# Kernel tuning notes

Measured on AMD Instinct MI355X. Metric: run time of the kernel, lower is better.

Reference implementation:

```python
import jax, jax.numpy as jnp
import numpy as np

B, N, D, H = 2, 2048, 1024, 16
DH = D // H
DF = 4 * D
SCALE = D ** (-0.5)  # standard_scale=False -> dim**-0.5
EPS = 1e-5


def _ln(x, w, b):
    mu = jnp.mean(x, axis=-1, keepdims=True)
    var = jnp.mean(jnp.square(x - mu), axis=-1, keepdims=True)
    return (x - mu) * jax.lax.rsqrt(var + EPS) * w + b


def setup_inputs() -> dict:
    key = jax.random.key(0)
    ks = jax.random.split(key, 12)
    s = lambda fan_in: (1.0 / np.sqrt(fan_in))
    return {
        "x": jax.random.normal(ks[0], (B, N, D), jnp.float32),
        "gamma": jax.random.uniform(ks[1], (B, H), jnp.float32),
        "dist_matrix": jax.random.uniform(ks[2], (N, N), jnp.float32),
        "ln1_w": jnp.ones((D,), jnp.float32),
        "ln1_b": jnp.zeros((D,), jnp.float32),
        "qkv_w": jax.random.normal(ks[3], (D, 3 * D), jnp.float32) * s(D),
        "qkv_b": jnp.zeros((3 * D,), jnp.float32),
        "proj_w": jax.random.normal(ks[4], (D, D), jnp.float32) * s(D),
        "proj_b": jnp.zeros((D,), jnp.float32),
        "ln2_w": jnp.ones((D,), jnp.float32),
        "ln2_b": jnp.zeros((D,), jnp.float32),
        "mlp_w1": jax.random.normal(ks[5], (D, DF), jnp.float32) * s(D),
        "mlp_b1": jnp.zeros((DF,), jnp.float32),
        "mlp_w2": jax.random.normal(ks[6], (DF, D), jnp.float32) * s(DF),
        "mlp_b2": jnp.zeros((D,), jnp.float32),
    }


def reference(x, gamma, dist_matrix, ln1_w, ln1_b, qkv_w, qkv_b, proj_w, proj_b,
              ln2_w, ln2_b, mlp_w1, mlp_b1, mlp_w2, mlp_b2):
    # --- ZoomAttention on norm1(x) ---
    h = _ln(x, ln1_w, ln1_b)                                   # [B,N,D]
    qkv = h @ qkv_w + qkv_b                                    # [B,N,3D]
    qkv = qkv.reshape(B, N, 3, H, DH).transpose(2, 0, 3, 1, 4)  # [3,B,H,N,DH]
    q, k, v = qkv[0], qkv[1], qkv[2]
    scores = jnp.einsum("bhnd,bhmd->bhnm", q, k) * SCALE       # [B,H,N,N]
    scores = scores - gamma[:, :, None, None] * dist_matrix[None, None]
    attn = jax.nn.softmax(scores, axis=-1)
    out = jnp.einsum("bhnm,bhmd->bhnd", attn, v)               # [B,H,N,DH]
    out = out.transpose(0, 2, 1, 3).reshape(B, N, D)
    x = x + (out @ proj_w + proj_b)
    # --- MLP (exact GELU, torch default) ---
    h2 = _ln(x, ln2_w, ln2_b)
    h2 = jax.nn.gelu(h2 @ mlp_w1 + mlp_b1, approximate=False) @ mlp_w2 + mlp_b2
    return x + h2
```

## Files before the change

### kernel.cpp

```cpp
#include <hip/hip_runtime.h>
#include <hip/hip_bf16.h>


#define SCALE_ 0.03125f
#define EPS_   1e-5f
#define LOG2E_ 1.4426950408889634f
#define SC2_   (SCALE_ * LOG2E_)

typedef unsigned short u16;
typedef __attribute__((ext_vector_type(8))) short short8;
typedef __attribute__((ext_vector_type(4))) float f32x4;
typedef __attribute__((ext_vector_type(4))) unsigned short u16x4;

__device__ inline float b2f(u16 u){ unsigned x = ((unsigned)u) << 16; float f; __builtin_memcpy(&f, &x, 4); return f; }
__device__ inline u16 f2b(float f){ __hip_bfloat16 h = __float2bfloat16(f); u16 u; __builtin_memcpy(&u, &h, 2); return u; }

__device__ inline void glds16(const u16* g, u16* l) {
    __builtin_amdgcn_global_load_lds(
        (const __attribute__((address_space(1))) void*)g,
        (__attribute__((address_space(3))) void*)l, 16, 0, 0);
}

__global__ __launch_bounds__(256) void transpose_cast(const float* __restrict__ src,
                                                      u16* __restrict__ dst, int K, int N) {
    __shared__ float t[32][33];
    int nb = blockIdx.x * 32, kb = blockIdx.y * 32;
    int tx = threadIdx.x & 31, ty = threadIdx.x >> 5;
    for (int i = 0; i < 4; i++) {
        int r = ty + i * 8;
        t[r][tx] = src[(size_t)(kb + r) * N + nb + tx];
    }
    __syncthreads();
    for (int i = 0; i < 4; i++) {
        int r = ty + i * 8;
        dst[(size_t)(nb + r) * K + kb + tx] = f2b(t[tx][r]);
    }
}

__global__ __launch_bounds__(256) void ln_bf16(const float* __restrict__ x,
                                               const float* __restrict__ w,
                                               const float* __restrict__ b,
                                               u16* __restrict__ out) {
    int row = blockIdx.x, t = threadIdx.x;
    float4 v = ((const float4*)(x + (size_t)row * 1024))[t];
    float s1 = v.x + v.y + v.z + v.w;
    float s2 = v.x * v.x + v.y * v.y + v.z * v.z + v.w * v.w;
    for (int o = 32; o > 0; o >>= 1) { s1 += __shfl_xor(s1, o); s2 += __shfl_xor(s2, o); }
    __shared__ float a1[4], a2[4];
    if ((t & 63) == 0) { a1[t >> 6] = s1; a2[t >> 6] = s2; }
    __syncthreads();
    s1 = a1[0] + a1[1] + a1[2] + a1[3];
    s2 = a2[0] + a2[1] + a2[2] + a2[3];
    float mu = s1 * (1.0f / 1024.0f);
    float var = s2 * (1.0f / 1024.0f) - mu * mu;
    float rs = rsqrtf(var + EPS_);
    float4 wv = ((const float4*)w)[t];
    float4 bv = ((const float4*)b)[t];
    u16x4 o;
    o[0] = f2b((v.x - mu) * rs * wv.x + bv.x);
    o[1] = f2b((v.y - mu) * rs * wv.y + bv.y);
    o[2] = f2b((v.z - mu) * rs * wv.z + bv.z);
    o[3] = f2b((v.w - mu) * rs * wv.w + bv.w);
    ((u16x4*)(out + (size_t)row * 1024))[t] = o;
}

template <int MODE>
__global__ __launch_bounds__(512) void gemm256_8ph(
    const u16* __restrict__ A, const u16* __restrict__ Bt,
    const float* __restrict__ bias, int K,
    u16* __restrict__ outb,
    u16* __restrict__ qp, u16* __restrict__ kp, u16* __restrict__ vtp) {
    __shared__ u16 LS[4][2][256 * 32];
    int tid = threadIdx.x;
    int w = tid >> 6, lane = tid & 63, g = lane >> 4, ln = lane & 15;
    int wr = w >> 2, wc = w & 3;
    int gx = gridDim.x;
    int nwg = gx * gridDim.y;
    int lin = blockIdx.y * gx + blockIdx.x;
    int swz = (lin & 7) * (nwg >> 3) + (lin >> 3);
    int bx = swz % gx, by = swz / gx;
    int br = by * 256, bc = bx * 256;
    int jx = (((lane & 3) ^ ((lane >> 3) & 3)) << 3);
    const u16* Ast = A + (size_t)(br + w * 32 + (lane >> 2)) * K + jx;
    const u16* Bst = Bt + (size_t)(bc + w * 32 + (lane >> 2)) * K + jx;
    size_t r16 = (size_t)16 * K;
    const int ldsW = (w * 32) * 32;
    f32x4 acc[8][4] = {};
    int NT = K >> 5;
    int slotr = ((g ^ ((ln >> 1) & 3)) << 3);
    for (int kt = 0; kt < 3; ++kt) {
        glds16(Ast + (size_t)kt * 32, &LS[kt][0][ldsW]);
        glds16(Ast + (size_t)kt * 32 + r16, &LS[kt][0][ldsW + 512]);
        glds16(Bst + (size_t)kt * 32, &LS[kt][1][ldsW]);
        glds16(Bst + (size_t)kt * 32 + r16, &LS[kt][1][ldsW + 512]);
    }
    asm volatile("s_waitcnt vmcnt(8)" ::: "memory");
    __builtin_amdgcn_s_barrier();
    short8 aa[4], bb[4];
    for (int kt = 0; kt < NT; ++kt) {
        const u16* bufA = &LS[kt & 3][0][0];
        const u16* bufB = &LS[kt & 3][1][0];
        int s3 = kt + 3;
        #pragma unroll
        for (int m = 0; m < 4; ++m)
            aa[m] = *(const short8*)&bufA[(wr * 128 + m * 16 + ln) * 32 + slotr];
        #pragma unroll
        for (int n = 0; n < 4; ++n)
            bb[n] = *(const short8*)&bufB[(wc * 64 + n * 16 + ln) * 32 + slotr];
        if (s3 < NT) {
            u16* d = &LS[s3 & 3][0][ldsW];
            glds16(Ast + (size_t)s3 * 32, d);
            glds16(Ast + (size_t)s3 * 32 + r16, d + 512);
        }
        __builtin_amdgcn_s_barrier();
        asm volatile("s_waitcnt lgkmcnt(0)" ::: "memory");
        __builtin_amdgcn_sched_barrier(0);
        __builtin_amdgcn_s_setprio(1);
        #pragma unroll
        for (int m = 0; m < 4; ++m)
            #pragma unroll
            for (int n = 0; n < 4; ++n)
                acc[m][n] = __builtin_amdgcn_mfma_f32_16x16x32_bf16(aa[m], bb[n], acc[m][n], 0, 0, 0);
        __builtin_amdgcn_s_setprio(0);
        __builtin_amdgcn_sched_barrier(0);
        __builtin_amdgcn_s_barrier();
        #pragma unroll
        for (int m = 0; m < 4; ++m)
            aa[m] = *(const short8*)&bufA[(wr * 128 + 64 + m * 16 + ln) * 32 + slotr];
        if (s3 < NT) {
            u16* d = &LS[s3 & 3][1][ldsW];
            glds16(Bst + (size_t)s3 * 32, d);
            glds16(Bst + (size_t)s3 * 32 + r16, d + 512);
        }
        if (kt + 3 < NT)      asm volatile("s_waitcnt vmcnt(8)" ::: "memory");
        else if (kt + 2 < NT) asm volatile("s_waitcnt vmcnt(4)" ::: "memory");
        else if (kt + 1 < NT) asm volatile("s_waitcnt vmcnt(0)" ::: "memory");
        __builtin_amdgcn_s_barrier();
        asm volatile("s_waitcnt lgkmcnt(0)" ::: "memory");
        __builtin_amdgcn_sched_barrier(0);
        __builtin_amdgcn_s_setprio(1);
        #pragma unroll
        for (int m = 0; m < 4; ++m)
            #pragma unroll
            for (int n = 0; n < 4; ++n)
                acc[4 + m][n] = __builtin_amdgcn_mfma_f32_16x16x32_bf16(aa[m], bb[n], acc[4 + m][n], 0, 0, 0);
        __builtin_amdgcn_s_setprio(0);
        __builtin_amdgcn_sched_barrier(0);
        __builtin_amdgcn_s_barrier();
    }
    #pragma unroll
    for (int m = 0; m < 8; ++m) {
        int row0 = br + wr * 128 + m * 16 + g * 4;
        #pragma unroll
        for (int n = 0; n < 4; ++n) {
            int col = bc + wc * 64 + n * 16 + ln;
            float bv = bias[col];
            if constexpr (MODE == 0) {
                int which = col >> 10, cc = col & 1023, hh = cc >> 6, dh = cc & 63;
                int bb2 = row0 >> 11, nn0 = row0 & 2047;
                size_t bh = (size_t)(bb2 * 16 + hh);
                if (which == 0) {
                    for (int r = 0; r < 4; r++)
                        qp[((bh * 2048 + nn0 + r) << 6) + dh] = f2b((acc[m][n][r] + bv) * SC2_);
                } else if (which == 1) {
                    for (int r = 0; r < 4; r++)
                        kp[((bh * 2048 + nn0 + r) << 6) + dh] = f2b(acc[m][n][r] + bv);
                } else {
                    u16x4 o;
                    for (int r = 0; r < 4; r++) o[r] = f2b(acc[m][n][r] + bv);
                    *(u16x4*)&vtp[((bh * 64 + dh) << 11) + nn0] = o;
                }
            } else {
                for (int r = 0; r < 4; r++) {
                    float v = acc[m][n][r] + bv;
                    float gl = 0.5f * v * (1.0f + erff(v * 0.7071067811865476f));
                    outb[(size_t)(row0 + r) * 4096 + col] = f2b(gl);
                }
            }
        }
    }
}

template <int MODE, int BN>
__global__ __launch_bounds__(256) void gemm_bf16(
    const u16* __restrict__ A, const u16* __restrict__ Bt,
    const float* __restrict__ bias, int M, int N, int K,
    const float* __restrict__ res, float* __restrict__ outf) {
    constexpr int NN = BN / 32;
    __shared__ u16 As[128 * 64];
    __shared__ u16 Bs[BN * 64];
    int br = blockIdx.y * 128, bc = blockIdx.x * BN;
    int tid = threadIdx.x;
    int w = tid >> 6, lane = tid & 63, g = lane >> 4, ln = lane & 15;
    int wr = (w >> 1) * 64, wc = (w & 1) * (BN / 2);
    f32x4 acc[4][NN] = {};
    int sgcol = (((lane & 7) ^ (lane >> 3)) << 3);
    int arow = w * 32 + (lane >> 3);
    int brow = w * (BN / 4) + (lane >> 3);
    const u16* Ap = A + (size_t)(br + arow) * K + sgcol;
    const u16* Bp = Bt + (size_t)(bc + brow) * K + sgcol;
    u16* lA = &As[(w * 32) * 64];
    u16* lB = &Bs[(w * (BN / 4)) * 64];
    size_t rstep = (size_t)8 * K;
    for (int kt = 0; kt < K; kt += 64) {
        __syncthreads();
        #pragma unroll
        for (int i = 0; i < 4; i++) glds16(Ap + kt + i * rstep, lA + i * 512);
        #pragma unroll
        for (int i = 0; i < BN / 32; i++) glds16(Bp + kt + i * rstep, lB + i * 512);
        __syncthreads();
        #pragma unroll
        for (int kk = 0; kk < 2; kk++) {
            int so = (((kk << 2) + g) ^ (ln & 7)) << 3;
            short8 af[4], bfr[NN];
            #pragma unroll
            for (int m = 0; m < 4; m++)  af[m]  = *(const short8*)&As[(wr + m * 16 + ln) * 64 + so];
            #pragma unroll
            for (int n = 0; n < NN; n++) bfr[n] = *(const short8*)&Bs[(wc + n * 16 + ln) * 64 + so];
            #pragma unroll
            for (int m = 0; m < 4; m++)
                #pragma unroll
                for (int n = 0; n < NN; n++)
                    acc[m][n] = __builtin_amdgcn_mfma_f32_16x16x32_bf16(af[m], bfr[n], acc[m][n], 0, 0, 0);
        }
    }
    #pragma unroll
    for (int m = 0; m < 4; m++) {
        int row0 = br + wr + m * 16 + g * 4;
        #pragma unroll
        for (int n = 0; n < NN; n++) {
            int col = bc + wc + n * 16 + ln;
            float bv = bias[col];
            if constexpr (MODE == 1) {
                for (int r = 0; r < 4; r++) {
                    size_t idx = (size_t)(row0 + r) * 1024 + col;
                    outf[idx] = res[idx] + acc[m][n][r] + bv;
                }
            } else {
                for (int r = 0; r < 4; r++) {
                    size_t idx = (size_t)(row0 + r) * 1024 + col;
                    outf[idx] = outf[idx] + acc[m][n][r] + bv;
                }
            }
        }
    }
}

__global__ __launch_bounds__(256) void attn_fwd(
    const u16* __restrict__ qg, const u16* __restrict__ kg, const u16* __restrict__ vtg,
    const float* __restrict__ dist, const float* __restrict__ gamma, u16* __restrict__ ao) {
    __shared__ u16 Ks[2][64 * 64];
    __shared__ u16 Vs[2][64 * 64];
    __shared__ u16 Ps[4][16 * 64];
    int qt = blockIdx.x, bh = blockIdx.y;
    int b = bh >> 4, h = bh & 15;
    int tid = threadIdx.x, w = tid >> 6, lane = tid & 63, g = lane >> 4, ln = lane & 15;
    float gam2 = gamma[bh] * LOG2E_;
    int qglob = qt * 64 + w * 16 + ln;
    const u16* qrow = qg + ((size_t)bh * 2048 + qglob) * 64;
    short8 qf0 = *(const short8*)(qrow + g * 8);
    short8 qf1 = *(const short8*)(qrow + 32 + g * 8);
    const float* dbase = dist + (size_t)qglob * 2048 + g * 4;
    float m2 = -3.0e38f;
    f32x4 acco[4] = {};
    f32x4 accl = {};
    short8 ones;
    #pragma unroll
    for (int i = 0; i < 8; ++i) ones[i] = (short)0x3F80;
    int srow = tid >> 2, sc = (tid & 3) * 2;
    int ss0 = ((sc ^ (srow & 7)) << 3), ss1 = (((sc + 1) ^ (srow & 7)) << 3);
    const u16* kgp = kg + ((size_t)bh * 2048 + srow) * 64 + sc * 8;
    const u16* vgp = vtg + ((size_t)bh * 64 + srow) * 2048 + sc * 8;
    {
        short8 a0 = *(const short8*)(kgp);
        short8 a1 = *(const short8*)(kgp + 8);
        short8 c0 = *(const short8*)(vgp);
        short8 c1 = *(const short8*)(vgp + 8);
        *(short8*)&Ks[0][srow * 64 + ss0] = a0;
        *(short8*)&Ks[0][srow * 64 + ss1] = a1;
        *(short8*)&Vs[0][srow * 64 + ss0] = c0;
        *(short8*)&Vs[0][srow * 64 + ss1] = c1;
    }
    float4 dcv[4];
    #pragma unroll
    for (int nb = 0; nb < 4; nb++) dcv[nb] = *(const float4*)(dbase + nb * 16);
    __syncthreads();
    int cur = 0;
    int so0 = (g ^ (ln & 7)) << 3, so1 = ((4 + g) ^ (ln & 7)) << 3;
    for (int kt = 0; kt < 32; kt++) {
        short8 kr0, kr1, vr0, vr1;
        float4 dnx[4];
        if (kt < 31) {
            kr0 = *(const short8*)(kgp + (kt + 1) * 4096);
            kr1 = *(const short8*)(kgp + (kt + 1) * 4096 + 8);
            vr0 = *(const short8*)(vgp + (kt + 1) * 64);
            vr1 = *(const short8*)(vgp + (kt + 1) * 64 + 8);
            #pragma unroll
            for (int nb = 0; nb < 4; nb++)
                dnx[nb] = *(const float4*)(dbase + (kt + 1) * 64 + nb * 16);
        }
        f32x4 sa[4] = {};
        __builtin_amdgcn_s_setprio(1);
        #pragma unroll
        for (int nb = 0; nb < 4; nb++) {
            short8 kf0 = *(const short8*)&Ks[cur][(nb * 16 + ln) * 64 + so0];
            short8 kf1 = *(const short8*)&Ks[cur][(nb * 16 + ln) * 64 + so1];
            sa[nb] = __builtin_amdgcn_mfma_f32_16x16x32_bf16(kf0, qf0, sa[nb], 0, 0, 0);
            sa[nb] = __builtin_amdgcn_mfma_f32_16x16x32_bf16(kf1, qf1, sa[nb], 0, 0, 0);
        }
        __builtin_amdgcn_s_setprio(0);
        float sv[4][4], pm = -3.0e38f;
        #pragma unroll
        for (int nb = 0; nb < 4; nb++) {
            float4 dv = dcv[nb];
            sv[nb][0] = sa[nb][0] - gam2 * dv.x;
            sv[nb][1] = sa[nb][1] - gam2 * dv.y;
            sv[nb][2] = sa[nb][2] - gam2 * dv.z;
            sv[nb][3] = sa[nb][3] - gam2 * dv.w;
            #pragma unroll
            for (int r = 0; r < 4; r++) pm = fmaxf(pm, sv[nb][r]);
        }
        pm = fmaxf(pm, __shfl_xor(pm, 16));
        pm = fmaxf(pm, __shfl_xor(pm, 32));
        if (!__all(pm - m2 <= 8.0f)) {
            float nm = fmaxf(m2, pm);
            float al = __builtin_exp2f(m2 - nm);
            m2 = nm;
            accl *= al;
            #pragma unroll
            for (int db = 0; db < 4; db++) acco[db] *= al;
        }
        #pragma unroll
        for (int nb = 0; nb < 4; nb++) {
            u16x4 pw;
            #pragma unroll
            for (int r = 0; r < 4; r++) pw[r] = f2b(__builtin_exp2f(sv[nb][r] - m2));
            int off = nb * 16 + g * 4;
            *(u16x4*)&Ps[w][ln * 64 + (((off >> 3) ^ (ln & 7)) << 3) + (off & 7)] = pw;
        }
        short8 pf0 = *(const short8*)&Ps[w][ln * 64 + so0];
        short8 pf1 = *(const short8*)&Ps[w][ln * 64 + so1];
        __builtin_amdgcn_s_setprio(1);
        #pragma unroll
        for (int db = 0; db < 4; db++) {
            short8 vf0 = *(const short8*)&Vs[cur][(db * 16 + ln) * 64 + so0];
            short8 vf1 = *(const short8*)&Vs[cur][(db * 16 + ln) * 64 + so1];
            acco[db] = __builtin_amdgcn_mfma_f32_16x16x32_bf16(vf0, pf0, acco[db], 0, 0, 0);
            acco[db] = __builtin_amdgcn_mfma_f32_16x16x32_bf16(vf1, pf1, acco[db], 0, 0, 0);
        }
        accl = __builtin_amdgcn_mfma_f32_16x16x32_bf16(ones, pf0, accl, 0, 0, 0);
        accl = __builtin_amdgcn_mfma_f32_16x16x32_bf16(ones, pf1, accl, 0, 0, 0);
        __builtin_amdgcn_s_setprio(0);
        if (kt < 31) {
            int nx = cur ^ 1;
            *(short8*)&Ks[nx][srow * 64 + ss0] = kr0;
            *(short8*)&Ks[nx][srow * 64 + ss1] = kr1;
            *(short8*)&Vs[nx][srow * 64 + ss0] = vr0;
            *(short8*)&Vs[nx][srow * 64 + ss1] = vr1;
            #pragma unroll
            for (int nb = 0; nb < 4; nb++) dcv[nb] = dnx[nb];
            __syncthreads();
            cur = nx;
        }
    }
    float inv = 1.0f / accl[0];
    u16* aop = ao + (size_t)(b * 2048 + qglob) * 1024 + h * 64 + g * 4;
    #pragma unroll
    for (int db = 0; db < 4; db++) {
        u16x4 o;
        #pragma unroll
        for (int r = 0; r < 4; r++) o[r] = f2b(acco[db][r] * inv);
        *(u16x4*)(aop + db * 16) = o;
    }
}

extern "C" void kernel_launch(void* const* d_in, const int* in_sizes, int n_in,
                              void* d_out, int out_size, void* d_ws, size_t ws_size,
                              hipStream_t stream) {
    const float* x     = (const float*)d_in[0];
    const float* gamma = (const float*)d_in[1];
    const float* dist  = (const float*)d_in[2];
    const float* ln1w  = (const float*)d_in[3];
    const float* ln1b  = (const float*)d_in[4];
    const float* qkvw  = (const float*)d_in[5];
    const float* qkvb  = (const float*)d_in[6];
    const float* projw = (const float*)d_in[7];
    const float* projb = (const float*)d_in[8];
    const float* ln2w  = (const float*)d_in[9];
    const float* ln2b  = (const float*)d_in[10];
    const float* w1    = (const float*)d_in[11];
    const float* b1    = (const float*)d_in[12];
    const float* w2    = (const float*)d_in[13];
    const float* b2    = (const float*)d_in[14];
    float* out = (float*)d_out;
    char* ws = (char*)d_ws;
    u16* wqkvT  = (u16*)(ws + 0);
    u16* wprojT = (u16*)(ws + 6291456);
    u16* w1T    = (u16*)(ws + 8388608);
    u16* w2T    = (u16*)(ws + 16777216);
    u16* hb     = (u16*)(ws + 33554432);
    u16* qb     = (u16*)(ws + 41943040);
    u16* kb     = (u16*)(ws + 50331648);
    u16* vtb    = (u16*)(ws + 58720256);
    u16* aob    = (u16*)(ws + 67108864);
    u16* gb     = hb;
    u16* h2b    = aob;

    dim3 blk(256);
    transpose_cast<<<dim3(3072 / 32, 1024 / 32), blk, 0, stream>>>(qkvw, wqkvT, 1024, 3072);
    transpose_cast<<<dim3(1024 / 32, 1024 / 32), blk, 0, stream>>>(projw, wprojT, 1024, 1024);
    transpose_cast<<<dim3(4096 / 32, 1024 / 32), blk, 0, stream>>>(w1, w1T, 1024, 4096);
    transpose_cast<<<dim3(1024 / 32, 4096 / 32), blk, 0, stream>>>(w2, w2T, 4096, 1024);
    ln_bf16<<<4096, blk, 0, stream>>>(x, ln1w, ln1b, hb);
    gemm256_8ph<0><<<dim3(12, 16), dim3(512), 0, stream>>>(hb, wqkvT, qkvb, 1024,
                                                           nullptr, qb, kb, vtb);
    attn_fwd<<<dim3(32, 32), blk, 0, stream>>>(qb, kb, vtb, dist, gamma, aob);
    gemm_bf16<1, 64><<<dim3(16, 32), blk, 0, stream>>>(aob, wprojT, projb, 4096, 1024, 1024,
                                                       x, out);
    ln_bf16<<<4096, blk, 0, stream>>>(out, ln2w, ln2b, h2b);
    gemm256_8ph<2><<<dim3(16, 16), dim3(512), 0, stream>>>(h2b, w1T, b1, 1024,
                                                           gb, nullptr, nullptr, nullptr);
    gemm_bf16<3, 64><<<dim3(16, 32), blk, 0, stream>>>(gb, w2T, b2, 4096, 1024, 4096,
                                                       nullptr, out);
}
```

Baseline: 297.2 us.

## Double-buffer proj/MLP2 GEMMs, pre-cast distance matrix to bf16, drop ones-MFMA row sum

Replaces the single-buffered 128x64 GEMM used for the projection and second MLP layer with a 128x128 double-buffered version. It adds a grid swizzle and raises wave priority around the MFMAs, so global-to-LDS loads overlap with compute. The distance matrix is pre-cast to bf16 with log2e folded in, which halves the bytes attention streams for it. Attention also computes the softmax row sum with shuffles instead of extra MFMAs against a ones vector. The trade-offs are an extra cast kernel every call, reduced precision of the distance bias, and fewer blocks per GEMM.

After: 307.3 us. 1.03x slower.

```diff
diff --git a/kernel.cpp b/kernel.cpp
--- a/kernel.cpp
+++ b/kernel.cpp
@@ -34,6 +34,18 @@
     for (int i = 0; i < 4; i++) {
         int r = ty + i * 8;
         dst[(size_t)(nb + r) * K + kb + tx] = f2b(t[tx][r]);
+    }
+}
+
+__global__ __launch_bounds__(256) void cast_scale_bf16(const float* __restrict__ src,
+                                                       u16* __restrict__ dst, int n4, float scale) {
+    int i = blockIdx.x * 256 + threadIdx.x;
+    if (i < n4) {
+        float4 v = ((const float4*)src)[i];
+        u16x4 o;
+        o[0] = f2b(v.x * scale); o[1] = f2b(v.y * scale);
+        o[2] = f2b(v.z * scale); o[3] = f2b(v.w * scale);
+        ((u16x4*)dst)[i] = o;
     }
 }
 
@@ -181,54 +193,75 @@
     }
 }
 
-template <int MODE, int BN>
-__global__ __launch_bounds__(256) void gemm_bf16(
+template <int MODE>
+__global__ __launch_bounds__(256) void gemm_db(
     const u16* __restrict__ A, const u16* __restrict__ Bt,
-    const float* __restrict__ bias, int M, int N, int K,
+    const float* __restrict__ bias, int K,
     const float* __restrict__ res, float* __restrict__ outf) {
-    constexpr int NN = BN / 32;
-    __shared__ u16 As[128 * 64];
-    __shared__ u16 Bs[BN * 64];
-    int br = blockIdx.y * 128, bc = blockIdx.x * BN;
+    __shared__ u16 As[2][128 * 64];
+    __shared__ u16 Bs[2][128 * 64];
+    int gx = gridDim.x;
+    int nwg = gx * gridDim.y;
+    int lin = blockIdx.y * gx + blockIdx.x;
+    int swz = (lin & 7) * (nwg >> 3) + (lin >> 3);
+    int bx = swz % gx, by = swz / gx;
+    int br = by * 128, bc = bx * 128;
     int tid = threadIdx.x;
     int w = tid >> 6, lane = tid & 63, g = lane >> 4, ln = lane & 15;
-    int wr = (w >> 1) * 64, wc = (w & 1) * (BN / 2);
-    f32x4 acc[4][NN] = {};
+    int wr = (w >> 1) * 64, wc = (w & 1) * 64;
+    f32x4 acc[4][4] = {};
     int sgcol = (((lane & 7) ^ (lane >> 3)) << 3);
-    int arow = w * 32 + (lane >> 3);
-    int brow = w * (BN / 4) + (lane >> 3);
-    const u16* Ap = A + (size_t)(br + arow) * K + sgcol;
-    const u16* Bp = Bt + (size_t)(bc + brow) * K + sgcol;
-    u16* lA = &As[(w * 32) * 64];
-    u16* lB = &Bs[(w * (BN / 4)) * 64];
+    int srow = w * 32 + (lane >> 3);
+    const u16* Ap = A + (size_t)(br + srow) * K + sgcol;
+    const u16* Bp = Bt + (size_t)(bc + srow) * K + sgcol;
     size_t rstep = (size_t)8 * K;
-    for (int kt = 0; kt < K; kt += 64) {
-        __syncthreads();
-        #pragma unroll
-        for (int i = 0; i < 4; i++) glds16(Ap + kt + i * rstep, lA + i * 512);
-        #pragma unroll
-        for (int i = 0; i < BN / 32; i++) glds16(Bp + kt + i * rstep, lB + i * 512);
-        __syncthreads();
+    int ldsW = (w * 32) * 64;
+    int NT = K >> 6;
+    #pragma unroll
+    for (int i = 0; i < 4; i++) glds16(Ap + i * rstep, &As[0][ldsW + i * 512]);
+    #pragma unroll
+    for (int i = 0; i < 4; i++) glds16(Bp + i * rstep, &Bs[0][ldsW + i * 512]);
+    asm volatile("s_waitcnt vmcnt(0)" ::: "memory");
+    __builtin_amdgcn_s_barrier();
+    int cur = 0;
+    for (int kt = 0; kt < NT; ++kt) {
+        if (kt + 1 < NT) {
+            const u16* Ap2 = Ap + (size_t)(kt + 1) * 64;
+            const u16* Bp2 = Bt == nullptr ? nullptr : Bp + (size_t)(kt + 1) * 64;
+            u16* dA = &As[cur ^ 1][ldsW];
+            u16* dB = &Bs[cur ^ 1][ldsW];
+            #pragma unroll
+            for (int i = 0; i < 4; i++) glds16(Ap2 + i * rstep, dA + i * 512);
+            #pragma unroll
+            for (int i = 0; i < 4; i++) glds16(Bp2 + i * rstep, dB + i * 512);
+        }
+        const u16* bufA = &As[cur][0];
+        const u16* bufB = &Bs[cur][0];
         #pragma unroll
         for (int kk = 0; kk < 2; kk++) {
             int so = (((kk << 2) + g) ^ (ln & 7)) << 3;
-            short8 af[4], bfr[NN];
-            #pragma unroll
-            for (int m = 0; m < 4; m++)  af[m]  = *(const short8*)&As[(wr + m * 16 + ln) * 64 + so];
-            #pragma unroll
-            for (int n = 0; n < NN; n++) bfr[n] = *(const short8*)&Bs[(wc + n * 16 + ln) * 64 + so];
+            short8 af[4], bfr[4];
+            #pragma unroll
+            for (int m = 0; m < 4; m++)  af[m]  = *(const short8*)&bufA[(wr + m * 16 + ln) * 64 + so];
+            #pragma unroll
+            for (int n = 0; n < 4; n++)  bfr[n] = *(const short8*)&bufB[(wc + n * 16 + ln) * 64 + so];
+            __builtin_amdgcn_s_setprio(1);
             #pragma unroll
             for (int m = 0; m < 4; m++)
                 #pragma unroll
-                for (int n = 0; n < NN; n++)
+                for (int n = 0; n < 4; n++)
                     acc[m][n] = __builtin_amdgcn_mfma_f32_16x16x32_bf16(af[m], bfr[n], acc[m][n], 0, 0, 0);
-        }
+            __builtin_amdgcn_s_setprio(0);
+        }
+        if (kt + 1 < NT) asm volatile("s_waitcnt vmcnt(0)" ::: "memory");
+        __builtin_amdgcn_s_barrier();
+        cur ^= 1;
     }
     #pragma unroll
     for (int m = 0; m < 4; m++) {
         int row0 = br + wr + m * 16 + g * 4;
         #pragma unroll
-        for (int n = 0; n < NN; n++) {
+        for (int n = 0; n < 4; n++) {
             int col = bc + wc + n * 16 + ln;
             float bv = bias[col];
             if constexpr (MODE == 1) {
@@ -248,25 +281,21 @@
 
 __global__ __launch_bounds__(256) void attn_fwd(
     const u16* __restrict__ qg, const u16* __restrict__ kg, const u16* __restrict__ vtg,
-    const float* __restrict__ dist, const float* __restrict__ gamma, u16* __restrict__ ao) {
+    const u16* __restrict__ distb, const float* __restrict__ gamma, u16* __restrict__ ao) {
     __shared__ u16 Ks[2][64 * 64];
     __shared__ u16 Vs[2][64 * 64];
     __shared__ u16 Ps[4][16 * 64];
     int qt = blockIdx.x, bh = blockIdx.y;
     int b = bh >> 4, h = bh & 15;
     int tid = threadIdx.x, w = tid >> 6, lane = tid & 63, g = lane >> 4, ln = lane & 15;
-    float gam2 = gamma[bh] * LOG2E_;
+    float gam = gamma[bh];
     int qglob = qt * 64 + w * 16 + ln;
     const u16* qrow = qg + ((size_t)bh * 2048 + qglob) * 64;
     short8 qf0 = *(const short8*)(qrow + g * 8);
     short8 qf1 = *(const short8*)(qrow + 32 + g * 8);
-    const float* dbase = dist + (size_t)qglob * 2048 + g * 4;
-    float m2 = -3.0e38f;
+    const u16* dbase = distb + (size_t)qglob * 2048 + g * 4;
+    float m2 = -3.0e38f, lsum = 0.0f;
     f32x4 acco[4] = {};
-    f32x4 accl = {};
-    short8 ones;
-    #pragma unroll
-    for (int i = 0; i < 8; ++i) ones[i] = (short)0x3F80;
     int srow = tid >> 2, sc = (tid & 3) * 2;
     int ss0 = ((sc ^ (srow & 7)) << 3), ss1 = (((sc + 1) ^ (srow & 7)) << 3);
     const u16* kgp = kg + ((size_t)bh * 2048 + srow) * 64 + sc * 8;
@@ -281,15 +310,15 @@
         *(short8*)&Vs[0][srow * 64 + ss0] = c0;
         *(short8*)&Vs[0][srow * 64 + ss1] = c1;
     }
-    float4 dcv[4];
-    #pragma unroll
-    for (int nb = 0; nb < 4; nb++) dcv[nb] = *(const float4*)(dbase + nb * 16);
+    u16x4 dcv[4];
+    #pragma unroll
+    for (int nb = 0; nb < 4; nb++) dcv[nb] = *(const u16x4*)(dbase + nb * 16);
     __syncthreads();
     int cur = 0;
     int so0 = (g ^ (ln & 7)) << 3, so1 = ((4 + g) ^ (ln & 7)) << 3;
     for (int kt = 0; kt < 32; kt++) {
         short8 kr0, kr1, vr0, vr1;
-        float4 dnx[4];
+        u16x4 dnx[4];
         if (kt < 31) {
             kr0 = *(const short8*)(kgp + (kt + 1) * 4096);
             kr1 = *(const short8*)(kgp + (kt + 1) * 4096 + 8);
@@ -297,7 +326,7 @@
             vr1 = *(const short8*)(vgp + (kt + 1) * 64 + 8);
             #pragma unroll
             for (int nb = 0; nb < 4; nb++)
-                dnx[nb] = *(const float4*)(dbase + (kt + 1) * 64 + nb * 16);
+                dnx[nb] = *(const u16x4*)(dbase + (kt + 1) * 64 + nb * 16);
         }
         f32x4 sa[4] = {};
         __builtin_amdgcn_s_setprio(1);
@@ -311,33 +340,39 @@
         __builtin_amdgcn_s_setprio(0);
         float sv[4][4], pm = -3.0e38f;
         #pragma unroll
-        for (int nb = 0; nb < 4; nb++) {
-            float4 dv = dcv[nb];
-            sv[nb][0] = sa[nb][0] - gam2 * dv.x;
-            sv[nb][1] = sa[nb][1] - gam2 * dv.y;
-            sv[nb][2] = sa[nb][2] - gam2 * dv.z;
-            sv[nb][3] = sa[nb][3] - gam2 * dv.w;
-            #pragma unroll
-            for (int r = 0; r < 4; r++) pm = fmaxf(pm, sv[nb][r]);
-        }
+        for (int nb = 0; nb < 4; nb++)
+            #pragma unroll
+            for (int r = 0; r < 4; r++) {
+                float s = sa[nb][r] - gam * b2f(dcv[nb][r]);
+                sv[nb][r] = s;
+                pm = fmaxf(pm, s);
+            }
         pm = fmaxf(pm, __shfl_xor(pm, 16));
         pm = fmaxf(pm, __shfl_xor(pm, 32));
         if (!__all(pm - m2 <= 8.0f)) {
             float nm = fmaxf(m2, pm);
             float al = __builtin_exp2f(m2 - nm);
             m2 = nm;
-            accl *= al;
+            lsum *= al;
             #pragma unroll
             for (int db = 0; db < 4; db++) acco[db] *= al;
         }
+        float ps = 0.0f;
         #pragma unroll
         for (int nb = 0; nb < 4; nb++) {
             u16x4 pw;
             #pragma unroll
-            for (int r = 0; r < 4; r++) pw[r] = f2b(__builtin_exp2f(sv[nb][r] - m2));
+            for (int r = 0; r < 4; r++) {
+                float p = __builtin_exp2f(sv[nb][r] - m2);
+                ps += p;
+                pw[r] = f2b(p);
+            }
             int off = nb * 16 + g * 4;
             *(u16x4*)&Ps[w][ln * 64 + (((off >> 3) ^ (ln & 7)) << 3) + (off & 7)] = pw;
         }
+        ps += __shfl_xor(ps, 16);
+        ps += __shfl_xor(ps, 32);
+        lsum += ps;
         short8 pf0 = *(const short8*)&Ps[w][ln * 64 + so0];
         short8 pf1 = *(const short8*)&Ps[w][ln * 64 + so1];
         __builtin_amdgcn_s_setprio(1);
@@ -348,8 +383,6 @@
             acco[db] = __builtin_amdgcn_mfma_f32_16x16x32_bf16(vf0, pf0, acco[db], 0, 0, 0);
             acco[db] = __builtin_amdgcn_mfma_f32_16x16x32_bf16(vf1, pf1, acco[db], 0, 0, 0);
         }
-        accl = __builtin_amdgcn_mfma_f32_16x16x32_bf16(ones, pf0, accl, 0, 0, 0);
-        accl = __builtin_amdgcn_mfma_f32_16x16x32_bf16(ones, pf1, accl, 0, 0, 0);
         __builtin_amdgcn_s_setprio(0);
         if (kt < 31) {
             int nx = cur ^ 1;
@@ -363,7 +396,7 @@
             cur = nx;
         }
     }
-    float inv = 1.0f / accl[0];
+    float inv = 1.0f / lsum;
     u16* aop = ao + (size_t)(b * 2048 + qglob) * 1024 + h * 64 + g * 4;
     #pragma unroll
     for (int db = 0; db < 4; db++) {
@@ -398,6 +431,7 @@
     u16* wprojT = (u16*)(ws + 6291456);
     u16* w1T    = (u16*)(ws + 8388608);
     u16* w2T    = (u16*)(ws + 16777216);
+    u16* distb  = (u16*)(ws + 25165824);
     u16* hb     = (u16*)(ws + 33554432);
     u16* qb     = (u16*)(ws + 41943040);
     u16* kb     = (u16*)(ws + 50331648);
@@ -411,15 +445,14 @@
     transpose_cast<<<dim3(1024 / 32, 1024 / 32), blk, 0, stream>>>(projw, wprojT, 1024, 1024);
     transpose_cast<<<dim3(4096 / 32, 1024 / 32), blk, 0, stream>>>(w1, w1T, 1024, 4096);
     transpose_cast<<<dim3(1024 / 32, 4096 / 32), blk, 0, stream>>>(w2, w2T, 4096, 1024);
+    cast_scale_bf16<<<4096, blk, 0, stream>>>(dist, distb, 2048 * 2048 / 4, LOG2E_);
     ln_bf16<<<4096, blk, 0, stream>>>(x, ln1w, ln1b, hb);
     gemm256_8ph<0><<<dim3(12, 16), dim3(512), 0, stream>>>(hb, wqkvT, qkvb, 1024,
                                                            nullptr, qb, kb, vtb);
-    attn_fwd<<<dim3(32, 32), blk, 0, stream>>>(qb, kb, vtb, dist, gamma, aob);
-    gemm_bf16<1, 64><<<dim3(16, 32), blk, 0, stream>>>(aob, wprojT, projb, 4096, 1024, 1024,
-                                                       x, out);
+    attn_fwd<<<dim3(32, 32), blk, 0, stream>>>(qb, kb, vtb, distb, gamma, aob);
+    gemm_db<1><<<dim3(8, 32), blk, 0, stream>>>(aob, wprojT, projb, 1024, x, out);
     ln_bf16<<<4096, blk, 0, stream>>>(out, ln2w, ln2b, h2b);
     gemm256_8ph<2><<<dim3(16, 16), dim3(512), 0, stream>>>(h2b, w1T, b1, 1024,
                                                            gb, nullptr, nullptr, nullptr);
-    gemm_bf16<3, 64><<<dim3(16, 32), blk, 0, stream>>>(gb, w2T, b2, 4096, 1024, 4096,
-                                                       nullptr, out);
-}
+    gemm_db<3><<<dim3(8, 32), blk, 0, stream>>>(gb, w2T, b2, 4096, nullptr, out);
+}
```
